# Optimization experiments

Hardware: AMD Instinct MI355X
Metric: run time of the kernel (lower is better)

## Reference

```python
import jax, jax.numpy as jnp
import numpy as np

EMBED_DIM = 512
NUM_HEADS = 8
HEAD_DIM = EMBED_DIM // NUM_HEADS
B, N = 2, 4096


def setup_inputs() -> dict:
    key = jax.random.key(0)
    ks = jax.random.split(key, 5)
    x = jax.random.normal(ks[0], (B, N, EMBED_DIM), dtype=jnp.float32)
    # causal mask: 1 where attention is allowed (j <= i), 0 elsewhere
    mask = jnp.tril(jnp.ones((N, N), dtype=jnp.int32))[None, None]  # [1,1,N,N]
    s_in = 1.0 / np.sqrt(EMBED_DIM)
    qkv_w = jax.random.uniform(ks[1], (3 * EMBED_DIM, EMBED_DIM), jnp.float32, -s_in, s_in)
    qkv_b = jax.random.uniform(ks[2], (3 * EMBED_DIM,), jnp.float32, -s_in, s_in)
    out_w = jax.random.uniform(ks[3], (EMBED_DIM, EMBED_DIM), jnp.float32, -s_in, s_in)
    out_b = jax.random.uniform(ks[4], (EMBED_DIM,), jnp.float32, -s_in, s_in)
    return {"x": x, "mask": mask, "qkv_w": qkv_w, "qkv_b": qkv_b,
            "out_w": out_w, "out_b": out_b}


def reference(x, mask, qkv_w, qkv_b, out_w, out_b):
    Bc, Nc, C = x.shape
    H, D = NUM_HEADS, HEAD_DIM
    scale = D ** (-0.5)
    qkv = x @ qkv_w.T + qkv_b                      # [B,N,3C]
    qkv = qkv.reshape(Bc, Nc, 3, H, D)
    q = jnp.transpose(qkv[:, :, 0], (0, 2, 1, 3))  # [B,H,N,D]
    k = jnp.transpose(qkv[:, :, 1], (0, 2, 1, 3))
    v = jnp.transpose(qkv[:, :, 2], (0, 2, 1, 3))
    scores = jnp.einsum('bhqd,bhkd->bhqk', q, k) * scale
    scores = jnp.where(mask == 0, -jnp.inf, scores)
    attn = jax.nn.softmax(scores, axis=-1)         # dropout p=0 (eval)
    out = jnp.einsum('bhqk,bhkd->bhqd', attn, v)   # [B,H,N,D]
    out = jnp.transpose(out, (0, 2, 1, 3)).reshape(Bc, Nc, C)
    return out @ out_w.T + out_b
```

## Files before the change

### kernel.cpp

```cpp
#include <hip/hip_runtime.h>
#include <hip/hip_bf16.h>
#include <cstdint>
#include <cstddef>

#define EMBED 512
#define NHEADS 8
#define HDIM 64
#define BATCH 2
#define SEQ 4096
#define TOKENS (BATCH*SEQ)
#define QSCALE 0.1803368801f

typedef __attribute__((ext_vector_type(8))) short short8;
typedef __attribute__((ext_vector_type(4))) float floatx4;

#if defined(__has_builtin)
# if __has_builtin(__builtin_amdgcn_exp2f)
#  define EXP2F(x) __builtin_amdgcn_exp2f(x)
# else
#  define EXP2F(x) exp2f(x)
# endif
#else
# define EXP2F(x) exp2f(x)
#endif

union U8 { uint4 u; short8 s; };

__device__ __forceinline__ unsigned short f2bf(float f){
  unsigned int u = __float_as_uint(f);
  u += 0x7fff + ((u >> 16) & 1);
  return (unsigned short)(u >> 16);
}

__device__ __forceinline__ unsigned int pkbf(float a, float b){
  unsigned int ra = __float_as_uint(a) + 0x8000u;
  unsigned int rb = __float_as_uint(b) + 0x8000u;
  return __builtin_amdgcn_perm(rb, ra, 0x07060302u);
}

__device__ __forceinline__ void gl2lds16(const unsigned short* g, unsigned short* l){
  __builtin_amdgcn_global_load_lds(
      (const __attribute__((address_space(1))) unsigned int*)g,
      (__attribute__((address_space(3))) unsigned int*)l, 16, 0, 0);
}

#define XN4  (TOKENS*EMBED/4)
#define W1N4 (3*EMBED*EMBED/4)
#define W2N4 (EMBED*EMBED/4)
__global__ void cvt_all(const float* __restrict__ x, const float* __restrict__ w1,
                        const float* __restrict__ w2, unsigned short* __restrict__ out){
  int i = blockIdx.x*blockDim.x + threadIdx.x;
  const float* s; int j;
  if (i < XN4){ s = x; j = i; }
  else if (i < XN4+W1N4){ s = w1; j = i - XN4; }
  else { s = w2; j = i - (XN4+W1N4); }
  float4 v = reinterpret_cast<const float4*>(s)[j];
  ushort4 o; o.x=f2bf(v.x); o.y=f2bf(v.y); o.z=f2bf(v.z); o.w=f2bf(v.w);
  reinterpret_cast<ushort4*>(out)[i] = o;
}

template<int MODE>
__global__ __launch_bounds__(256) void gemm_bt(
    const unsigned short* __restrict__ A,
    const unsigned short* __restrict__ Bw,
    const float* __restrict__ bias,
    unsigned short* __restrict__ Qb,
    unsigned short* __restrict__ Kb,
    unsigned short* __restrict__ Vb,
    float* __restrict__ Cout)
{
  const int K = EMBED;
  __shared__ unsigned short Al[2][128*64];
  __shared__ unsigned short Bl[2][128*64];
  const int tm = blockIdx.x * 128;
  const int tn = blockIdx.y * 128;
  const int tid = threadIdx.x;
  const int w = tid >> 6, lane = tid & 63;
  const int m16 = lane & 15, q4 = lane >> 4;
  const int wm = w & 1, wn = w >> 1;
  const bool transp = (MODE == 1) || (tn < 2*EMBED);

  floatx4 acc[4][4];
  #pragma unroll
  for (int i=0;i<4;i++)
    #pragma unroll
    for (int j=0;j<4;j++) acc[i][j] = (floatx4){0.f,0.f,0.f,0.f};

  const int srow = tid >> 3, p8 = tid & 7, c8 = p8 ^ (srow & 7);

  auto stage = [&](int k0, int buf){
    #pragma unroll
    for (int cal=0; cal<4; cal++){
      gl2lds16(A  + (size_t)(tm + cal*32 + srow)*K + k0 + c8*8, &Al[buf][cal*2048 + tid*8]);
      gl2lds16(Bw + (size_t)(tn + cal*32 + srow)*K + k0 + c8*8, &Bl[buf][cal*2048 + tid*8]);
    }
  };

  stage(0, 0);
  for (int k0 = 0; k0 < K; k0 += 64){
    const int cur = (k0 >> 6) & 1;
    __syncthreads();
    if (k0 + 64 < K) stage(k0 + 64, cur^1);
    short8 af[4][2], bfv[4][2];
    #pragma unroll
    for (int i=0;i<4;i++)
      #pragma unroll
      for (int s=0;s<2;s++)
        af[i][s] = *reinterpret_cast<const short8*>(&Al[cur][(wm*64 + i*16 + m16)*64 + (((s*4+q4) ^ (m16&7))*8)]);
    #pragma unroll
    for (int j=0;j<4;j++)
      #pragma unroll
      for (int s=0;s<2;s++)
        bfv[j][s] = *reinterpret_cast<const short8*>(&Bl[cur][(wn*64 + j*16 + m16)*64 + (((s*4+q4) ^ (m16&7))*8)]);
    #pragma unroll
    for (int i=0;i<4;i++)
      #pragma unroll
      for (int j=0;j<4;j++)
        #pragma unroll
        for (int s=0;s<2;s++){
          if (transp)
            acc[i][j] = __builtin_amdgcn_mfma_f32_16x16x32_bf16(bfv[j][s], af[i][s], acc[i][j], 0,0,0);
          else
            acc[i][j] = __builtin_amdgcn_mfma_f32_16x16x32_bf16(af[i][s], bfv[j][s], acc[i][j], 0,0,0);
        }
  }

  if (MODE == 1){
    #pragma unroll
    for (int j=0;j<4;j++){
      const int col0 = tn + wn*64 + j*16 + q4*4;
      const float4 bv = *reinterpret_cast<const float4*>(bias + col0);
      #pragma unroll
      for (int i=0;i<4;i++){
        const int row = tm + wm*64 + i*16 + m16;
        float4 o;
        o.x = acc[i][j][0] + bv.x; o.y = acc[i][j][1] + bv.y;
        o.z = acc[i][j][2] + bv.z; o.w = acc[i][j][3] + bv.w;
        *reinterpret_cast<float4*>(Cout + (size_t)row*EMBED + col0) = o;
      }
    }
    return;
  }

  if (transp){
    #pragma unroll
    for (int j=0;j<4;j++){
      const int col0 = tn + wn*64 + j*16 + q4*4;
      const int which = col0 >> 9, h = (col0 >> 6) & 7, d0 = col0 & 63;
      const float4 bv = *reinterpret_cast<const float4*>(bias + col0);
      #pragma unroll
      for (int i=0;i<4;i++){
        const int row = tm + wm*64 + i*16 + m16;
        const int b = row >> 12, n = row & (SEQ-1);
        float v0 = acc[i][j][0] + bv.x, v1 = acc[i][j][1] + bv.y;
        float v2 = acc[i][j][2] + bv.z, v3 = acc[i][j][3] + bv.w;
        unsigned short* dst;
        if (which == 0){
          v0 *= QSCALE; v1 *= QSCALE; v2 *= QSCALE; v3 *= QSCALE;
          dst = Qb + ((size_t)(b*NHEADS + h)*SEQ + n)*HDIM + d0;
        } else {
          dst = Kb + ((size_t)(b*NHEADS + h)*SEQ + n)*HDIM + d0;
        }
        uint2 pk; pk.x = pkbf(v0, v1); pk.y = pkbf(v2, v3);
        *reinterpret_cast<uint2*>(dst) = pk;
      }
    }
  } else {
    #pragma unroll
    for (int j=0;j<4;j++){
      const int col = tn + wn*64 + j*16 + m16;
      const float bv = bias[col];
      const int h = (col >> 6) & 7, d = col & 63;
      #pragma unroll
      for (int i=0;i<4;i++){
        const int row0 = tm + wm*64 + i*16 + q4*4;
        const int b = row0 >> 12, n0 = row0 & (SEQ-1);
        uint2 pk;
        pk.x = pkbf(acc[i][j][0] + bv, acc[i][j][1] + bv);
        pk.y = pkbf(acc[i][j][2] + bv, acc[i][j][3] + bv);
        *reinterpret_cast<uint2*>(Vb + ((size_t)(b*NHEADS + h)*HDIM + d)*SEQ + n0) = pk;
      }
    }
  }
}

__global__ __launch_bounds__(256, 4) void flash_attn(
  const unsigned short* __restrict__ Qb,
  const unsigned short* __restrict__ Kb,
  const unsigned short* __restrict__ Vb,
  unsigned short* __restrict__ Ob)
{
  __shared__ unsigned short KVl[2][2*64*64];

  const int blk = blockIdx.x;
  const int qt = (blk < 512) ? (63 - (blk >> 4)) : ((blk >> 4) - 32);
  const int bh = blk & 15;
  const int qbase = qt * 64;
  const unsigned short* Qh = Qb + (size_t)bh*SEQ*HDIM;
  const unsigned short* Kh = Kb + (size_t)bh*SEQ*HDIM;
  const unsigned short* Vh = Vb + (size_t)bh*HDIM*SEQ;

  const int tid = threadIdx.x, w = tid>>6, lane = tid&63;
  const int m16 = lane & 15, q4 = lane >> 4;
  const int srow = tid >> 3, p8 = tid & 7, c8 = p8 ^ (srow & 7);
  const int x7 = m16 & 7;
  const int kprow = 8*((srow>>2)&3) + 4*(srow>>4) + (srow&3);

  short8 ones;
  #pragma unroll
  for (int i=0;i<8;i++) ones[i] = (short)0x3F80;

  const int rowg0 = qbase + w*16;
  short8 qf0, qf1;
  {
    const unsigned short* qp = Qh + (size_t)(rowg0 + m16)*HDIM + q4*8;
    qf0 = *reinterpret_cast<const short8*>(qp);
    qf1 = *reinterpret_cast<const short8*>(qp + 32);
  }

  floatx4 oacc[4];
  floatx4 lacc = (floatx4){0.f,0.f,0.f,0.f};
  #pragma unroll
  for (int t=0;t<4;t++) oacc[t] = (floatx4){0.f,0.f,0.f,0.f};

  const unsigned short* ks = Kh + (size_t)kprow*HDIM + c8*8;
  const unsigned short* vs = Vh + (size_t)srow*SEQ + c8*8;

  gl2lds16(ks,            &KVl[0][tid*8]);
  gl2lds16(ks + 32*HDIM,  &KVl[0][32*64 + tid*8]);
  gl2lds16(vs,            &KVl[0][64*64 + tid*8]);
  gl2lds16(vs + 32*SEQ,   &KVl[0][64*64 + 32*64 + tid*8]);
  ks += 64*HDIM; vs += 64;

  const int key8 = 8*q4;
  for (int jt = 0; jt <= qt; jt++){
    const int cur = jt & 1;
    const int jbase = jt*64;
    __syncthreads();
    if (jt < qt){
      unsigned short* dst = &KVl[cur^1][0];
      gl2lds16(ks,           dst + tid*8);
      gl2lds16(ks + 32*HDIM, dst + 32*64 + tid*8);
      gl2lds16(vs,           dst + 64*64 + tid*8);
      gl2lds16(vs + 32*SEQ,  dst + 64*64 + 32*64 + tid*8);
      ks += 64*HDIM; vs += 64;
    }
    if (jbase > rowg0 + 15) continue;
    const unsigned short* Kl = &KVl[cur][0];
    const unsigned short* Vl = &KVl[cur][64*64];

    floatx4 s[4];
    #pragma unroll
    for (int t=0;t<4;t++){
      floatx4 a = (floatx4){0.f,0.f,0.f,0.f};
      short8 kf0 = *reinterpret_cast<const short8*>(Kl + (t*16 + m16)*64 + ((q4     ^ x7)*8));
      short8 kf1 = *reinterpret_cast<const short8*>(Kl + (t*16 + m16)*64 + (((q4+4) ^ x7)*8));
      a = __builtin_amdgcn_mfma_f32_16x16x32_bf16(kf0, qf0, a, 0,0,0);
      a = __builtin_amdgcn_mfma_f32_16x16x32_bf16(kf1, qf1, a, 0,0,0);
      s[t] = a;
    }

    if (jbase + 63 > rowg0){
      #pragma unroll
      for (int t=0;t<4;t++){
        const int kb = ((t>>1)<<5) + ((t&1)<<2);
        #pragma unroll
        for (int r=0;r<4;r++){
          float p = EXP2F(s[t][r]);
          const int key = jbase + kb + key8 + r;
          if (key > rowg0 + m16) p = 0.f;
          s[t][r] = p;
        }
      }
    } else {
      #pragma unroll
      for (int t=0;t<4;t++)
        #pragma unroll
        for (int r=0;r<4;r++)
          s[t][r] = EXP2F(s[t][r]);
    }

    short8 pf[2];
    #pragma unroll
    for (int tp=0; tp<2; tp++){
      U8 a;
      a.u.x = pkbf(s[2*tp][0],   s[2*tp][1]);
      a.u.y = pkbf(s[2*tp][2],   s[2*tp][3]);
      a.u.z = pkbf(s[2*tp+1][0], s[2*tp+1][1]);
      a.u.w = pkbf(s[2*tp+1][2], s[2*tp+1][3]);
      pf[tp] = a.s;
    }

    lacc = __builtin_amdgcn_mfma_f32_16x16x32_bf16(pf[0], ones, lacc, 0,0,0);
    lacc = __builtin_amdgcn_mfma_f32_16x16x32_bf16(pf[1], ones, lacc, 0,0,0);

    #pragma unroll
    for (int dt=0; dt<4; dt++){
      const unsigned short* vrow = Vl + (dt*16 + m16)*64;
      #pragma unroll
      for (int tp=0; tp<2; tp++){
        short8 vf = *reinterpret_cast<const short8*>(vrow + (((4*tp + q4) ^ x7)*8));
        oacc[dt] = __builtin_amdgcn_mfma_f32_16x16x32_bf16(pf[tp], vf, oacc[dt], 0,0,0);
      }
    }
  }

  const int b = bh >> 3, h = bh & 7;
  #pragma unroll
  for (int r=0;r<4;r++){
    const float inv = 1.0f / lacc[r];
    const int n = rowg0 + q4*4 + r;
    const size_t base = ((size_t)(b*SEQ + n))*EMBED + h*HDIM;
    #pragma unroll
    for (int t=0;t<4;t++)
      Ob[base + t*16 + m16] = f2bf(oacc[t][r] * inv);
  }
}

extern "C" void kernel_launch(void* const* d_in, const int* in_sizes, int n_in,
                              void* d_out, int out_size, void* d_ws, size_t ws_size,
                              hipStream_t stream){
  const float* x      = (const float*)d_in[0];
  const float* qkv_w  = (const float*)d_in[2];
  const float* qkv_b  = (const float*)d_in[3];
  const float* out_w  = (const float*)d_in[4];
  const float* out_b  = (const float*)d_in[5];
  float* out = (float*)d_out;

  unsigned short* ws = (unsigned short*)d_ws;
  unsigned short* xb  = ws;
  unsigned short* qwb = xb  + (size_t)TOKENS*EMBED;
  unsigned short* owb = qwb + (size_t)3*EMBED*EMBED;
  unsigned short* Qb  = owb + (size_t)EMBED*EMBED;
  unsigned short* Kb  = Qb  + (size_t)BATCH*NHEADS*SEQ*HDIM;
  unsigned short* Vb  = Kb  + (size_t)BATCH*NHEADS*SEQ*HDIM;
  unsigned short* Ob  = Vb  + (size_t)BATCH*NHEADS*SEQ*HDIM;

  cvt_all<<<dim3((XN4+W1N4+W2N4)/256), 256, 0, stream>>>(x, qkv_w, out_w, xb);
  gemm_bt<0><<<dim3(TOKENS/128, 3*EMBED/128), 256, 0, stream>>>(xb, qwb, qkv_b, Qb, Kb, Vb, nullptr);
  flash_attn<<<dim3(SEQ/64*16), 256, 0, stream>>>(Qb, Kb, Vb, Ob);
  gemm_bt<1><<<dim3(TOKENS/128, EMBED/128), 256, 0, stream>>>(Ob, owb, out_b, nullptr, nullptr, nullptr, out);
}
```

Measured before the change: 201.5 us.

## Use two-wave attention blocks with each wave handling two 16-row query tiles

The flash attention block shrinks from four waves to two, and each wave now processes two 16-row query sub-tiles (rows w*16 and w*16+32). K fragments loaded from LDS are reused across both row tiles, and each V fragment feeds two MFMAs. The KV staging is reworked for 128 threads with eight async copies per tile. This halves LDS reads per MFMA and per-block thread count, at the cost of more registers per wave and fewer waves available for latency hiding. The causal skip per wave is replaced by masking only on the diagonal tile.

```diff
diff --git a/kernel.cpp b/kernel.cpp
--- a/kernel.cpp
+++ b/kernel.cpp
@@ -184,7 +184,7 @@
   }
 }
 
-__global__ __launch_bounds__(256, 4) void flash_attn(
+__global__ __launch_bounds__(128, 2) void flash_attn(
   const unsigned short* __restrict__ Qb,
   const unsigned short* __restrict__ Kb,
   const unsigned short* __restrict__ Vb,
@@ -204,95 +204,108 @@
   const int m16 = lane & 15, q4 = lane >> 4;
   const int srow = tid >> 3, p8 = tid & 7, c8 = p8 ^ (srow & 7);
   const int x7 = m16 & 7;
-  const int kprow = 8*((srow>>2)&3) + 4*(srow>>4) + (srow&3);
+  const int kprow = 8*((srow>>2)&3) + (srow&3);
 
   short8 ones;
   #pragma unroll
   for (int i=0;i<8;i++) ones[i] = (short)0x3F80;
 
   const int rowg0 = qbase + w*16;
-  short8 qf0, qf1;
-  {
-    const unsigned short* qp = Qh + (size_t)(rowg0 + m16)*HDIM + q4*8;
-    qf0 = *reinterpret_cast<const short8*>(qp);
-    qf1 = *reinterpret_cast<const short8*>(qp + 32);
-  }
-
-  floatx4 oacc[4];
-  floatx4 lacc = (floatx4){0.f,0.f,0.f,0.f};
-  #pragma unroll
-  for (int t=0;t<4;t++) oacc[t] = (floatx4){0.f,0.f,0.f,0.f};
+  short8 qf[2][2];
+  #pragma unroll
+  for (int rt=0; rt<2; rt++){
+    const unsigned short* qp = Qh + (size_t)(rowg0 + rt*32 + m16)*HDIM + q4*8;
+    qf[rt][0] = *reinterpret_cast<const short8*>(qp);
+    qf[rt][1] = *reinterpret_cast<const short8*>(qp + 32);
+  }
+
+  floatx4 oacc[2][4];
+  floatx4 lacc[2] = {(floatx4){0.f,0.f,0.f,0.f}, (floatx4){0.f,0.f,0.f,0.f}};
+  #pragma unroll
+  for (int rt=0;rt<2;rt++)
+    #pragma unroll
+    for (int t=0;t<4;t++) oacc[rt][t] = (floatx4){0.f,0.f,0.f,0.f};
 
   const unsigned short* ks = Kh + (size_t)kprow*HDIM + c8*8;
   const unsigned short* vs = Vh + (size_t)srow*SEQ + c8*8;
 
-  gl2lds16(ks,            &KVl[0][tid*8]);
-  gl2lds16(ks + 32*HDIM,  &KVl[0][32*64 + tid*8]);
-  gl2lds16(vs,            &KVl[0][64*64 + tid*8]);
-  gl2lds16(vs + 32*SEQ,   &KVl[0][64*64 + 32*64 + tid*8]);
-  ks += 64*HDIM; vs += 64;
+  auto stageKV = [&](unsigned short* dst){
+    gl2lds16(ks,            dst + tid*8);
+    gl2lds16(ks + 4*HDIM,   dst + 16*64 + tid*8);
+    gl2lds16(ks + 32*HDIM,  dst + 32*64 + tid*8);
+    gl2lds16(ks + 36*HDIM,  dst + 48*64 + tid*8);
+    gl2lds16(vs,            dst + 64*64 + tid*8);
+    gl2lds16(vs + 16*SEQ,   dst + 64*64 + 16*64 + tid*8);
+    gl2lds16(vs + 32*SEQ,   dst + 64*64 + 32*64 + tid*8);
+    gl2lds16(vs + 48*SEQ,   dst + 64*64 + 48*64 + tid*8);
+    ks += 64*HDIM; vs += 64;
+  };
+
+  stageKV(&KVl[0][0]);
 
   const int key8 = 8*q4;
   for (int jt = 0; jt <= qt; jt++){
     const int cur = jt & 1;
     const int jbase = jt*64;
     __syncthreads();
-    if (jt < qt){
-      unsigned short* dst = &KVl[cur^1][0];
-      gl2lds16(ks,           dst + tid*8);
-      gl2lds16(ks + 32*HDIM, dst + 32*64 + tid*8);
-      gl2lds16(vs,           dst + 64*64 + tid*8);
-      gl2lds16(vs + 32*SEQ,  dst + 64*64 + 32*64 + tid*8);
-      ks += 64*HDIM; vs += 64;
-    }
-    if (jbase > rowg0 + 15) continue;
+    if (jt < qt) stageKV(&KVl[cur^1][0]);
     const unsigned short* Kl = &KVl[cur][0];
     const unsigned short* Vl = &KVl[cur][64*64];
-
-    floatx4 s[4];
+    const bool diag = (jt == qt);
+
+    short8 kf[4][2];
     #pragma unroll
     for (int t=0;t<4;t++){
-      floatx4 a = (floatx4){0.f,0.f,0.f,0.f};
-      short8 kf0 = *reinterpret_cast<const short8*>(Kl + (t*16 + m16)*64 + ((q4     ^ x7)*8));
-      short8 kf1 = *reinterpret_cast<const short8*>(Kl + (t*16 + m16)*64 + (((q4+4) ^ x7)*8));
-      a = __builtin_amdgcn_mfma_f32_16x16x32_bf16(kf0, qf0, a, 0,0,0);
-      a = __builtin_amdgcn_mfma_f32_16x16x32_bf16(kf1, qf1, a, 0,0,0);
-      s[t] = a;
-    }
-
-    if (jbase + 63 > rowg0){
+      kf[t][0] = *reinterpret_cast<const short8*>(Kl + (t*16 + m16)*64 + ((q4     ^ x7)*8));
+      kf[t][1] = *reinterpret_cast<const short8*>(Kl + (t*16 + m16)*64 + (((q4+4) ^ x7)*8));
+    }
+
+    short8 pf[2][2];
+    #pragma unroll
+    for (int rt=0; rt<2; rt++){
+      const int rowr = rowg0 + rt*32;
+      floatx4 s[4];
       #pragma unroll
       for (int t=0;t<4;t++){
-        const int kb = ((t>>1)<<5) + ((t&1)<<2);
+        floatx4 a = (floatx4){0.f,0.f,0.f,0.f};
+        a = __builtin_amdgcn_mfma_f32_16x16x32_bf16(kf[t][0], qf[rt][0], a, 0,0,0);
+        a = __builtin_amdgcn_mfma_f32_16x16x32_bf16(kf[t][1], qf[rt][1], a, 0,0,0);
+        s[t] = a;
+      }
+
+      if (diag){
         #pragma unroll
-        for (int r=0;r<4;r++){
-          float p = EXP2F(s[t][r]);
-          const int key = jbase + kb + key8 + r;
-          if (key > rowg0 + m16) p = 0.f;
-          s[t][r] = p;
+        for (int t=0;t<4;t++){
+          const int kb = ((t>>1)<<5) + ((t&1)<<2);
+          #pragma unroll
+          for (int r=0;r<4;r++){
+            float p = EXP2F(s[t][r]);
+            const int key = jbase + kb + key8 + r;
+            if (key > rowr + m16) p = 0.f;
+            s[t][r] = p;
+          }
         }
-      }
-    } else {
-      #pragma unroll
-      for (int t=0;t<4;t++)
+      } else {
         #pragma unroll
-        for (int r=0;r<4;r++)
-          s[t][r] = EXP2F(s[t][r]);
-    }
-
-    short8 pf[2];
-    #pragma unroll
-    for (int tp=0; tp<2; tp++){
-      U8 a;
-      a.u.x = pkbf(s[2*tp][0],   s[2*tp][1]);
-      a.u.y = pkbf(s[2*tp][2],   s[2*tp][3]);
-      a.u.z = pkbf(s[2*tp+1][0], s[2*tp+1][1]);
-      a.u.w = pkbf(s[2*tp+1][2], s[2*tp+1][3]);
-      pf[tp] = a.s;
-    }
-
-    lacc = __builtin_amdgcn_mfma_f32_16x16x32_bf16(pf[0], ones, lacc, 0,0,0);
-    lacc = __builtin_amdgcn_mfma_f32_16x16x32_bf16(pf[1], ones, lacc, 0,0,0);
+        for (int t=0;t<4;t++)
+          #pragma unroll
+          for (int r=0;r<4;r++)
+            s[t][r] = EXP2F(s[t][r]);
+      }
+
+      #pragma unroll
+      for (int tp=0; tp<2; tp++){
+        U8 a;
+        a.u.x = pkbf(s[2*tp][0],   s[2*tp][1]);
+        a.u.y = pkbf(s[2*tp][2],   s[2*tp][3]);
+        a.u.z = pkbf(s[2*tp+1][0], s[2*tp+1][1]);
+        a.u.w = pkbf(s[2*tp+1][2], s[2*tp+1][3]);
+        pf[rt][tp] = a.s;
+      }
+
+      lacc[rt] = __builtin_amdgcn_mfma_f32_16x16x32_bf16(pf[rt][0], ones, lacc[rt], 0,0,0);
+      lacc[rt] = __builtin_amdgcn_mfma_f32_16x16x32_bf16(pf[rt][1], ones, lacc[rt], 0,0,0);
+    }
 
     #pragma unroll
     for (int dt=0; dt<4; dt++){
@@ -300,20 +313,24 @@
       #pragma unroll
       for (int tp=0; tp<2; tp++){
         short8 vf = *reinterpret_cast<const short8*>(vrow + (((4*tp + q4) ^ x7)*8));
-        oacc[dt] = __builtin_amdgcn_mfma_f32_16x16x32_bf16(pf[tp], vf, oacc[dt], 0,0,0);
+        oacc[0][dt] = __builtin_amdgcn_mfma_f32_16x16x32_bf16(pf[0][tp], vf, oacc[0][dt], 0,0,0);
+        oacc[1][dt] = __builtin_amdgcn_mfma_f32_16x16x32_bf16(pf[1][tp], vf, oacc[1][dt], 0,0,0);
       }
     }
   }
 
   const int b = bh >> 3, h = bh & 7;
   #pragma unroll
-  for (int r=0;r<4;r++){
-    const float inv = 1.0f / lacc[r];
-    const int n = rowg0 + q4*4 + r;
-    const size_t base = ((size_t)(b*SEQ + n))*EMBED + h*HDIM;
-    #pragma unroll
-    for (int t=0;t<4;t++)
-      Ob[base + t*16 + m16] = f2bf(oacc[t][r] * inv);
+  for (int rt=0; rt<2; rt++){
+    #pragma unroll
+    for (int r=0;r<4;r++){
+      const float inv = 1.0f / lacc[rt][r];
+      const int n = rowg0 + rt*32 + q4*4 + r;
+      const size_t base = ((size_t)(b*SEQ + n))*EMBED + h*HDIM;
+      #pragma unroll
+      for (int t=0;t<4;t++)
+        Ob[base + t*16 + m16] = f2bf(oacc[rt][t][r] * inv);
+    }
   }
 }
 
@@ -338,6 +355,6 @@
 
   cvt_all<<<dim3((XN4+W1N4+W2N4)/256), 256, 0, stream>>>(x, qkv_w, out_w, xb);
   gemm_bt<0><<<dim3(TOKENS/128, 3*EMBED/128), 256, 0, stream>>>(xb, qwb, qkv_b, Qb, Kb, Vb, nullptr);
-  flash_attn<<<dim3(SEQ/64*16), 256, 0, stream>>>(Qb, Kb, Vb, Ob);
+  flash_attn<<<dim3(SEQ/64*16), 128, 0, stream>>>(Qb, Kb, Vb, Ob);
   gemm_bt<1><<<dim3(TOKENS/128, EMBED/128), 256, 0, stream>>>(Ob, owb, out_b, nullptr, nullptr, nullptr, out);
 }
```

After: 214.5 us. 6.5% more time.
